# Performance work log

Hardware: AMD Instinct MI355X
Metric: run time of the kernel (lower is better)

The kernel has to match this reference:

```python
import jax, jax.numpy as jnp
import numpy as np

B, S_IMG, S_TXT, D, H, HD = 1, 4096, 512, 3072, 24, 128
EPS = 1e-5
SCALE = 1.0 / np.sqrt(HD)


def _linear(x, W, b=None):
    # torch nn.Linear: y = x @ W.T + b, W is [out, in]
    y = jnp.einsum('bsd,od->bso', x, W)
    return y if b is None else y + b


def _rmsnorm(x, w):
    # over last dim (head_dim), torch nn.RMSNorm with affine weight
    var = jnp.mean(jnp.square(x), axis=-1, keepdims=True)
    return x * jax.lax.rsqrt(var + EPS) * w


def _rope(x, cos, sin):
    # x: [B, S, H, D]; cos/sin: [S, D]; interleaved-pair rotation
    xr = x.reshape(*x.shape[:-1], HD // 2, 2)
    x_real, x_imag = xr[..., 0], xr[..., 1]
    x_rot = jnp.stack([-x_imag, x_real], axis=-1).reshape(x.shape)
    return x * cos[None, :, None, :] + x_rot * sin[None, :, None, :]


def setup_inputs() -> dict:
    key = jax.random.key(0)
    ks = jax.random.split(key, 24)
    s = 0.02
    inp = {
        'hidden_states': jax.random.normal(ks[0], (B, S_IMG, D), jnp.float32),
        'encoder_hidden_states': jax.random.normal(ks[1], (B, S_TXT, D), jnp.float32),
        'rope_cos': jax.random.uniform(ks[2], (S_IMG + S_TXT, HD), jnp.float32),
        'rope_sin': jax.random.uniform(ks[3], (S_IMG + S_TXT, HD), jnp.float32),
        # image-stream qkv (bias=False)
        'Wq': jax.random.normal(ks[4], (D, D), jnp.float32) * s,
        'Wk': jax.random.normal(ks[5], (D, D), jnp.float32) * s,
        'Wv': jax.random.normal(ks[6], (D, D), jnp.float32) * s,
        # text-stream qkv (bias=True)
        'Waq': jax.random.normal(ks[7], (D, D), jnp.float32) * s,
        'baq': jnp.zeros((D,), jnp.float32),
        'Wak': jax.random.normal(ks[8], (D, D), jnp.float32) * s,
        'bak': jnp.zeros((D,), jnp.float32),
        'Wav': jax.random.normal(ks[9], (D, D), jnp.float32) * s,
        'bav': jnp.zeros((D,), jnp.float32),
        # output projections (bias=True)
        'Wo': jax.random.normal(ks[10], (D, D), jnp.float32) * s,
        'bo': jnp.zeros((D,), jnp.float32),
        'Wao': jax.random.normal(ks[11], (D, D), jnp.float32) * s,
        'bao': jnp.zeros((D,), jnp.float32),
        # RMSNorm weights on head_dim
        'wq_norm': jnp.ones((HD,), jnp.float32),
        'wk_norm': jnp.ones((HD,), jnp.float32),
        'waq_norm': jnp.ones((HD,), jnp.float32),
        'wak_norm': jnp.ones((HD,), jnp.float32),
    }
    return inp


def reference(hidden_states, encoder_hidden_states, rope_cos, rope_sin,
              Wq, Wk, Wv, Waq, baq, Wak, bak, Wav, bav,
              Wo, bo, Wao, bao, wq_norm, wk_norm, waq_norm, wak_norm):
    # image-stream qkv -> [B, S_img, H, HD]
    q = _linear(hidden_states, Wq).reshape(B, S_IMG, H, HD)
    k = _linear(hidden_states, Wk).reshape(B, S_IMG, H, HD)
    v = _linear(hidden_states, Wv).reshape(B, S_IMG, H, HD)
    q = _rmsnorm(q, wq_norm)
    k = _rmsnorm(k, wk_norm)
    # text-stream qkv -> [B, S_txt, H, HD]
    eq = _linear(encoder_hidden_states, Waq, baq).reshape(B, S_TXT, H, HD)
    ek = _linear(encoder_hidden_states, Wak, bak).reshape(B, S_TXT, H, HD)
    ev = _linear(encoder_hidden_states, Wav, bav).reshape(B, S_TXT, H, HD)
    eq = _rmsnorm(eq, waq_norm)
    ek = _rmsnorm(ek, wak_norm)
    # concat [encoder, image] along sequence
    q = jnp.concatenate([eq, q], axis=1)  # [B, S_total, H, HD]
    k = jnp.concatenate([ek, k], axis=1)
    v = jnp.concatenate([ev, v], axis=1)
    # RoPE on joint sequence
    q = _rope(q, rope_cos, rope_sin)
    k = _rope(k, rope_cos, rope_sin)
    # SDPA over joint sequence
    scores = jnp.einsum('bqhd,bkhd->bhqk', q, k) * SCALE
    probs = jax.nn.softmax(scores, axis=-1)
    out = jnp.einsum('bhqk,bkhd->bqhd', probs, v)  # [B, S_total, H, HD]
    out = out.reshape(B, S_IMG + S_TXT, D)
    enc_out = _linear(out[:, :S_TXT], Wao, bao)
    img_out = _linear(out[:, S_TXT:], Wo, bo)
    return (img_out, enc_out)
```

## Files before the change

### kernel.cpp

```cpp
#include <hip/hip_runtime.h>

typedef __bf16 bf16_t;
typedef __bf16 bf16x8 __attribute__((ext_vector_type(8)));
typedef float  f32x4  __attribute__((ext_vector_type(4)));

#define S_IMG 4096
#define S_TXT 512
#define S_TOT 4608
#define DMODEL 3072
#define NH 24
#define HD 128

__device__ __forceinline__ void load_lds16(const void* g, void* l) {
  __builtin_amdgcn_global_load_lds(
      (const __attribute__((address_space(1))) void*)g,
      (__attribute__((address_space(3))) void*)l, 16, 0, 0);
}

#define BARRIER() do { asm volatile("" ::: "memory");                          \
                       __builtin_amdgcn_s_barrier();                           \
                       asm volatile("" ::: "memory"); } while (0)

__global__ __launch_bounds__(256) void f2b_kernel(const float* __restrict__ in,
                                                  bf16_t* __restrict__ out, int n) {
  int i = (blockIdx.x * 256 + threadIdx.x) * 4;
  if (i >= n) return;
  float4 v = *(const float4*)(in + i);
  union { bf16_t b[4]; uint2 u; } pk;
  pk.b[0] = (bf16_t)v.x; pk.b[1] = (bf16_t)v.y;
  pk.b[2] = (bf16_t)v.z; pk.b[3] = (bf16_t)v.w;
  *(uint2*)(out + i) = pk.u;
}

template <typename OT>
__global__ __launch_bounds__(512, 2) void gemm256(
    const bf16_t* __restrict__ A0, const bf16_t* __restrict__ B0,
    OT* __restrict__ C0, const float* __restrict__ bias0, int mt0,
    const bf16_t* __restrict__ A1, const bf16_t* __restrict__ B1,
    OT* __restrict__ C1, const float* __restrict__ bias1, int swzq)
{
  const int NT = DMODEL / 64;
  __shared__ bf16_t As[2][2][256 * 32];
  __shared__ bf16_t Bs[2][2][256 * 32];

  int bid = blockIdx.x;
  int t = (bid & 7) * swzq + (bid >> 3);
  int nb0 = mt0 * 12;
  const bf16_t* A; const bf16_t* B; OT* C; const float* bias;
  if (t < nb0) { A = A0; B = B0; C = C0; bias = bias0; }
  else { t -= nb0; A = A1; B = B1; C = C1; bias = bias1; }
  int bx = t % 12, by = t / 12;

  int tid = threadIdx.x;
  int lane = tid & 63, wid = tid >> 6;
  int l15 = lane & 15, lg = lane >> 4;
  int wm = wid >> 2, wn = wid & 3;

  const bf16_t* Ag = A + (size_t)by * 256 * DMODEL;
  const bf16_t* Bg = B + (size_t)bx * 256 * DMODEL;

  int ur0 = tid >> 2;
  int uc0 = (tid & 3) * 8;

  auto stage = [&](int ht) {
    int T = ht >> 2, sl = ht & 3, kh = sl >> 1;
    const bf16_t* G = (sl & 1) ? Bg : Ag;
    bf16_t* L = (sl & 1) ? &Bs[T & 1][kh][0] : &As[T & 1][kh][0];
    int kbase = T * 64 + kh * 32;
    #pragma unroll
    for (int j = 0; j < 2; j++) {
      int r = j * 128 + ur0;
      load_lds16(G + (size_t)r * DMODEL + kbase + uc0,
                 (char*)L + (size_t)(j * 512 + tid) * 16);
    }
  };

  f32x4 acc[8][4];
  f32x4 zero = {0.f, 0.f, 0.f, 0.f};
  #pragma unroll
  for (int m = 0; m < 8; m++)
    #pragma unroll
    for (int n = 0; n < 4; n++) acc[m][n] = zero;

  stage(0); stage(1); stage(2); stage(3); stage(4); stage(5);
  asm volatile("s_waitcnt vmcnt(8)" ::: "memory");
  BARRIER();

  for (int T = 0; T < NT; ++T) {
    int cur = T & 1;
    const bf16_t* A0s = &As[cur][0][0];
    const bf16_t* A1s = &As[cur][1][0];
    const bf16_t* B0s = &Bs[cur][0][0];
    const bf16_t* B1s = &Bs[cur][1][0];
    bf16x8 af[4], bfr[4];

    #pragma unroll
    for (int n = 0; n < 4; n++)
      bfr[n] = *(const bf16x8*)(B0s + (wn * 64 + n * 16 + l15) * 32 + lg * 8);
    #pragma unroll
    for (int m = 0; m < 4; m++)
      af[m] = *(const bf16x8*)(A0s + (wm * 128 + m * 16 + l15) * 32 + lg * 8);
    if (T + 1 < NT) stage(4 * T + 6);
    BARRIER();
    __builtin_amdgcn_s_setprio(1);
    #pragma unroll
    for (int m = 0; m < 4; m++)
      #pragma unroll
      for (int n = 0; n < 4; n++)
        acc[m][n] = __builtin_amdgcn_mfma_f32_16x16x32_bf16(af[m], bfr[n], acc[m][n], 0, 0, 0);
    __builtin_amdgcn_s_setprio(0);
    BARRIER();

    #pragma unroll
    for (int m = 0; m < 4; m++)
      af[m] = *(const bf16x8*)(A0s + (wm * 128 + 64 + m * 16 + l15) * 32 + lg * 8);
    if (T + 1 < NT) stage(4 * T + 7);
    BARRIER();
    __builtin_amdgcn_s_setprio(1);
    #pragma unroll
    for (int m = 0; m < 4; m++)
      #pragma unroll
      for (int n = 0; n < 4; n++)
        acc[4 + m][n] = __builtin_amdgcn_mfma_f32_16x16x32_bf16(af[m], bfr[n], acc[4 + m][n], 0, 0, 0);
    __builtin_amdgcn_s_setprio(0);
    if (T < NT - 1) asm volatile("s_waitcnt vmcnt(8)" ::: "memory");
    else            asm volatile("s_waitcnt vmcnt(0)" ::: "memory");
    BARRIER();

    #pragma unroll
    for (int n = 0; n < 4; n++)
      bfr[n] = *(const bf16x8*)(B1s + (wn * 64 + n * 16 + l15) * 32 + lg * 8);
    #pragma unroll
    for (int m = 0; m < 4; m++)
      af[m] = *(const bf16x8*)(A1s + (wm * 128 + m * 16 + l15) * 32 + lg * 8);
    if (T + 2 < NT) stage(4 * T + 8);
    BARRIER();
    __builtin_amdgcn_s_setprio(1);
    #pragma unroll
    for (int m = 0; m < 4; m++)
      #pragma unroll
      for (int n = 0; n < 4; n++)
        acc[m][n] = __builtin_amdgcn_mfma_f32_16x16x32_bf16(af[m], bfr[n], acc[m][n], 0, 0, 0);
    __builtin_amdgcn_s_setprio(0);
    BARRIER();

    #pragma unroll
    for (int m = 0; m < 4; m++)
      af[m] = *(const bf16x8*)(A1s + (wm * 128 + 64 + m * 16 + l15) * 32 + lg * 8);
    if (T + 2 < NT) stage(4 * T + 9);
    BARRIER();
    __builtin_amdgcn_s_setprio(1);
    #pragma unroll
    for (int m = 0; m < 4; m++)
      #pragma unroll
      for (int n = 0; n < 4; n++)
        acc[4 + m][n] = __builtin_amdgcn_mfma_f32_16x16x32_bf16(af[m], bfr[n], acc[4 + m][n], 0, 0, 0);
    __builtin_amdgcn_s_setprio(0);
    if (T < NT - 2)      asm volatile("s_waitcnt vmcnt(8)" ::: "memory");
    else if (T == NT - 2) asm volatile("s_waitcnt vmcnt(4)" ::: "memory");
    BARRIER();
  }

  size_t row0 = (size_t)by * 256 + wm * 128;
  int col0 = bx * 256 + wn * 64;
  #pragma unroll
  for (int n = 0; n < 4; n++) {
    int col = col0 + n * 16 + l15;
    float bv = bias ? bias[col] : 0.f;
    #pragma unroll
    for (int m = 0; m < 8; m++) {
      #pragma unroll
      for (int r = 0; r < 4; r++) {
        size_t row = row0 + m * 16 + lg * 4 + r;
        C[row * DMODEL + col] = (OT)(acc[m][n][r] + bv);
      }
    }
  }
}

__global__ __launch_bounds__(256) void qk_post(
    const bf16_t* __restrict__ qbuf, const bf16_t* __restrict__ kbuf,
    const float* __restrict__ cosb, const float* __restrict__ sinb,
    const float* __restrict__ wqn, const float* __restrict__ wkn,
    const float* __restrict__ waqn, const float* __restrict__ wakn,
    bf16_t* __restrict__ Qh, bf16_t* __restrict__ Kh)
{
  int gw = blockIdx.x * 4 + (threadIdx.x >> 6);
  int lane = threadIdx.x & 63;
  int s = gw / NH, h = gw - (gw / NH) * NH;
  if (s >= S_TOT) return;
  int d0 = lane * 2;
  const bf16_t* qp = qbuf + (size_t)s * DMODEL + h * HD + d0;
  const bf16_t* kp = kbuf + (size_t)s * DMODEL + h * HD + d0;
  float q0 = (float)qp[0], q1 = (float)qp[1];
  float k0 = (float)kp[0], k1 = (float)kp[1];
  float sq = q0 * q0 + q1 * q1, sk = k0 * k0 + k1 * k1;
  #pragma unroll
  for (int m = 1; m < 64; m <<= 1) { sq += __shfl_xor(sq, m); sk += __shfl_xor(sk, m); }
  float rq = rsqrtf(sq * (1.f / HD) + 1e-5f);
  float rk = rsqrtf(sk * (1.f / HD) + 1e-5f);
  const float* qn = (s < S_TXT) ? waqn : wqn;
  const float* kn = (s < S_TXT) ? wakn : wkn;
  q0 *= rq * qn[d0]; q1 *= rq * qn[d0 + 1];
  k0 *= rk * kn[d0]; k1 *= rk * kn[d0 + 1];
  float c0 = cosb[s * HD + d0], c1 = cosb[s * HD + d0 + 1];
  float s0 = sinb[s * HD + d0], s1 = sinb[s * HD + d0 + 1];
  const float SCALE = 0.1275174319942397f;
  float oq0 = (q0 * c0 - q1 * s0) * SCALE;
  float oq1 = (q1 * c1 + q0 * s1) * SCALE;
  float ok0 = k0 * c0 - k1 * s0;
  float ok1 = k1 * c1 + k0 * s1;
  size_t ob = ((size_t)h * S_TOT + s) * HD + d0;
  union { bf16_t b[2]; unsigned int u; } pq, pk;
  pq.b[0] = (bf16_t)oq0; pq.b[1] = (bf16_t)oq1;
  pk.b[0] = (bf16_t)ok0; pk.b[1] = (bf16_t)ok1;
  *(unsigned int*)(Qh + ob) = pq.u;
  *(unsigned int*)(Kh + ob) = pk.u;
}

__global__ __launch_bounds__(256) void v_trans(const bf16_t* __restrict__ vbuf,
                                               bf16_t* __restrict__ Vt) {
  __shared__ bf16_t tile[64 * 130];
  int h = blockIdx.y, s0 = blockIdx.x * 64;
  int tid = threadIdx.x;
  #pragma unroll
  for (int i = 0; i < 16; i++) {
    int idx = tid + i * 256;
    int sr = idx >> 6, dp = idx & 63;
    unsigned int u = *(const unsigned int*)(vbuf + (size_t)(s0 + sr) * DMODEL + h * HD + dp * 2);
    *(unsigned int*)&tile[sr * 130 + dp * 2] = u;
  }
  __syncthreads();
  #pragma unroll
  for (int i = 0; i < 16; i++) {
    int idx = tid + i * 256;
    int d = idx >> 5, scp = idx & 31;
    union { bf16_t b[2]; unsigned int u; } pk;
    pk.b[0] = tile[(scp * 2) * 130 + d];
    pk.b[1] = tile[(scp * 2 + 1) * 130 + d];
    *(unsigned int*)(Vt + ((size_t)h * HD + d) * S_TOT + s0 + scp * 2) = pk.u;
  }
}

__global__ __launch_bounds__(256, 2) void attn_kernel(
    const bf16_t* __restrict__ Qh, const bf16_t* __restrict__ Kh,
    const bf16_t* __restrict__ Vt, bf16_t* __restrict__ O)
{
  int bid = blockIdx.x;
  int orig = (bid & 7) * 108 + (bid >> 3);
  int h = orig / 36;
  int q0 = (orig % 36) * 128;

  int tid = threadIdx.x, w = tid >> 6, lane = tid & 63;
  int l15 = lane & 15, lg = lane >> 4;
  int sw = (l15 & 7) << 4;

  __shared__ bf16_t Ks[2][64 * 128];
  __shared__ bf16_t Vs[2][128 * 64];
  __shared__ bf16_t Ps[4][32 * 64];

  const bf16_t* Kbase = Kh + (size_t)h * S_TOT * HD;
  const bf16_t* Vbase = Vt + (size_t)h * HD * S_TOT;
  bf16_t* Pw = &Ps[w][0];

  bf16x8 qf[2][4];
  #pragma unroll
  for (int qh = 0; qh < 2; qh++) {
    const bf16_t* Qrow = Qh + ((size_t)h * S_TOT + q0 + w * 32 + qh * 16 + l15) * HD + lg * 8;
    #pragma unroll
    for (int dc = 0; dc < 4; dc++) qf[qh][dc] = *(const bf16x8*)(Qrow + dc * 32);
  }

  f32x4 o[2][8];
  f32x4 zero = {0.f, 0.f, 0.f, 0.f};
  #pragma unroll
  for (int qh = 0; qh < 2; qh++)
    #pragma unroll
    for (int i = 0; i < 8; i++) o[qh][i] = zero;
  float m0 = -1e30f, m1 = -1e30f, l0 = 0.f, l1 = 0.f;

#define STAGE(buf, kt) do {                                                    \
    _Pragma("unroll")                                                          \
    for (int i_ = 0; i_ < 4; i_++) {                                           \
      int Lb = (tid + i_ * 256) * 16; int row = Lb >> 8, cb = Lb & 255;        \
      int sb = cb ^ ((row & 7) << 4);                                          \
      load_lds16(Kbase + (size_t)((kt) + row) * HD + (sb >> 1),                \
                 (char*)Ks[buf] + Lb);                                         \
    }                                                                          \
    _Pragma("unroll")                                                          \
    for (int i_ = 0; i_ < 4; i_++) {                                           \
      int Lb = (tid + i_ * 256) * 16; int row = Lb >> 7, cb = Lb & 127;        \
      int sb = cb ^ ((row & 7) << 4);                                          \
      load_lds16(Vbase + (size_t)row * S_TOT + (kt) + (sb >> 1),               \
                 (char*)Vs[buf] + Lb);                                         \
    }                                                                          \
  } while (0)

  STAGE(0, 0);
  __syncthreads();

  const int NT = S_TOT / 64;
  for (int t = 0; t < NT; ++t) {
    int cur = t & 1;
    if (t + 1 < NT) STAGE(cur ^ 1, (t + 1) * 64);

    f32x4 sacc[2][4];
    #pragma unroll
    for (int qh = 0; qh < 2; qh++)
      #pragma unroll
      for (int c = 0; c < 4; c++) sacc[qh][c] = zero;
    const char* Kc = (const char*)Ks[cur];
    #pragma unroll
    for (int c = 0; c < 4; c++) {
      int row = c * 16 + l15;
      int rs = (row & 7) << 4;
      const char* kr = Kc + row * 256;
      #pragma unroll
      for (int dc = 0; dc < 4; dc++) {
        bf16x8 kf = *(const bf16x8*)(kr + ((dc * 64 + lg * 16) ^ rs));
        sacc[0][c] = __builtin_amdgcn_mfma_f32_16x16x32_bf16(kf, qf[0][dc], sacc[0][c], 0, 0, 0);
        sacc[1][c] = __builtin_amdgcn_mfma_f32_16x16x32_bf16(kf, qf[1][dc], sacc[1][c], 0, 0, 0);
      }
    }

    float px0 = sacc[0][0][0], px1 = sacc[1][0][0];
    #pragma unroll
    for (int c = 0; c < 4; c++)
      #pragma unroll
      for (int r = 0; r < 4; r++) {
        px0 = fmaxf(px0, sacc[0][c][r]);
        px1 = fmaxf(px1, sacc[1][c][r]);
      }
    px0 = fmaxf(px0, __shfl_xor(px0, 16)); px0 = fmaxf(px0, __shfl_xor(px0, 32));
    px1 = fmaxf(px1, __shfl_xor(px1, 16)); px1 = fmaxf(px1, __shfl_xor(px1, 32));

    bool need = (px0 > m0 + 8.f) || (px1 > m1 + 8.f);
    if (__any(need)) {
      float mn0 = fmaxf(m0, px0), mn1 = fmaxf(m1, px1);
      float a0 = exp2f(m0 - mn0), a1 = exp2f(m1 - mn1);
      m0 = mn0; m1 = mn1; l0 *= a0; l1 *= a1;
      #pragma unroll
      for (int r = 0; r < 4; r++) {
        float f0 = __shfl(a0, lg * 4 + r);
        float f1 = __shfl(a1, lg * 4 + r);
        #pragma unroll
        for (int dn = 0; dn < 8; dn++) { o[0][dn][r] *= f0; o[1][dn][r] *= f1; }
      }
    }

    #pragma unroll
    for (int qh = 0; qh < 2; qh++) {
      float m = qh ? m1 : m0;
      float rsum = 0.f;
      char* Prow = (char*)Pw + (qh * 16 + l15) * 128;
      #pragma unroll
      for (int c = 0; c < 4; c++) {
        union { bf16_t b[4]; uint2 u; } pk;
        #pragma unroll
        for (int r = 0; r < 4; r++) {
          float p = exp2f(sacc[qh][c][r] - m);
          rsum += p;
          pk.b[r] = (bf16_t)p;
        }
        *(uint2*)(Prow + ((c * 32 + lg * 8) ^ sw)) = pk.u;
      }
      rsum += __shfl_xor(rsum, 16);
      rsum += __shfl_xor(rsum, 32);
      if (qh) l1 += rsum; else l0 += rsum;
    }

    bf16x8 pf[2][2];
    #pragma unroll
    for (int qh = 0; qh < 2; qh++) {
      const char* Prow = (const char*)Pw + (qh * 16 + l15) * 128;
      #pragma unroll
      for (int kc = 0; kc < 2; kc++)
        pf[qh][kc] = *(const bf16x8*)(Prow + ((kc * 64 + lg * 16) ^ sw));
    }
    const char* Vc = (const char*)Vs[cur];
    #pragma unroll
    for (int dn = 0; dn < 8; dn++) {
      int row = dn * 16 + l15;
      int rs2 = (row & 7) << 4;
      const char* vr = Vc + row * 128;
      bf16x8 vf0 = *(const bf16x8*)(vr + ((lg * 16) ^ rs2));
      bf16x8 vf1 = *(const bf16x8*)(vr + ((64 + lg * 16) ^ rs2));
      o[0][dn] = __builtin_amdgcn_mfma_f32_16x16x32_bf16(pf[0][0], vf0, o[0][dn], 0, 0, 0);
      o[0][dn] = __builtin_amdgcn_mfma_f32_16x16x32_bf16(pf[0][1], vf1, o[0][dn], 0, 0, 0);
      o[1][dn] = __builtin_amdgcn_mfma_f32_16x16x32_bf16(pf[1][0], vf0, o[1][dn], 0, 0, 0);
      o[1][dn] = __builtin_amdgcn_mfma_f32_16x16x32_bf16(pf[1][1], vf1, o[1][dn], 0, 0, 0);
    }

    __syncthreads();
  }
#undef STAGE

  #pragma unroll
  for (int qh = 0; qh < 2; qh++) {
    #pragma unroll
    for (int r = 0; r < 4; r++) {
      float lv = __shfl(qh ? l1 : l0, lg * 4 + r);
      float inv = 1.f / lv;
      size_t srow = (size_t)q0 + w * 32 + qh * 16 + lg * 4 + r;
      #pragma unroll
      for (int dn = 0; dn < 8; dn++)
        O[srow * DMODEL + h * HD + dn * 16 + l15] = (bf16_t)(o[qh][dn][r] * inv);
    }
  }
}

extern "C" void kernel_launch(void* const* d_in, const int* in_sizes, int n_in,
                              void* d_out, int out_size, void* d_ws, size_t ws_size,
                              hipStream_t stream) {
  const float* hidden = (const float*)d_in[0];
  const float* enc    = (const float*)d_in[1];
  const float* ropec  = (const float*)d_in[2];
  const float* ropes  = (const float*)d_in[3];
  const float* Wq  = (const float*)d_in[4];
  const float* Wk  = (const float*)d_in[5];
  const float* Wv  = (const float*)d_in[6];
  const float* Waq = (const float*)d_in[7];
  const float* baq = (const float*)d_in[8];
  const float* Wak = (const float*)d_in[9];
  const float* bak = (const float*)d_in[10];
  const float* Wav = (const float*)d_in[11];
  const float* bav = (const float*)d_in[12];
  const float* Wo  = (const float*)d_in[13];
  const float* bo  = (const float*)d_in[14];
  const float* Wao = (const float*)d_in[15];
  const float* bao = (const float*)d_in[16];
  const float* wqn = (const float*)d_in[17];
  const float* wkn = (const float*)d_in[18];
  const float* waqn = (const float*)d_in[19];
  const float* wakn = (const float*)d_in[20];

  const size_t WSZ = (size_t)DMODEL * DMODEL;
  const size_t SEQSZ = (size_t)S_TOT * DMODEL;
  if (ws_size < (2 * WSZ + 6 * SEQSZ) * sizeof(bf16_t)) return;

  bf16_t* s0   = (bf16_t*)d_ws;
  bf16_t* s1   = s0 + WSZ;
  bf16_t* xbi  = s1 + WSZ;
  bf16_t* xbt  = xbi + (size_t)S_IMG * DMODEL;
  bf16_t* qbuf = xbi + SEQSZ;
  bf16_t* kbuf = qbuf + SEQSZ;
  bf16_t* vbuf = kbuf + SEQSZ;
  bf16_t* Kh   = vbuf + SEQSZ;
  bf16_t* Vh   = Kh + SEQSZ;
  bf16_t* Qh   = xbi;
  bf16_t* attn_o = qbuf;
  float* outf = (float*)d_out;

  f2b_kernel<<<S_IMG * DMODEL / 1024, 256, 0, stream>>>(hidden, xbi, S_IMG * DMODEL);
  f2b_kernel<<<S_TXT * DMODEL / 1024, 256, 0, stream>>>(enc, xbt, S_TXT * DMODEL);

  const int WB = (int)(WSZ / 1024);
  f2b_kernel<<<WB, 256, 0, stream>>>(Wq,  s0, (int)WSZ);
  f2b_kernel<<<WB, 256, 0, stream>>>(Waq, s1, (int)WSZ);
  gemm256<bf16_t><<<216, 512, 0, stream>>>(
      xbi, s0, qbuf + (size_t)S_TXT * DMODEL, nullptr, 16,
      xbt, s1, qbuf, baq, 27);
  f2b_kernel<<<WB, 256, 0, stream>>>(Wk,  s0, (int)WSZ);
  f2b_kernel<<<WB, 256, 0, stream>>>(Wak, s1, (int)WSZ);
  gemm256<bf16_t><<<216, 512, 0, stream>>>(
      xbi, s0, kbuf + (size_t)S_TXT * DMODEL, nullptr, 16,
      xbt, s1, kbuf, bak, 27);
  f2b_kernel<<<WB, 256, 0, stream>>>(Wv,  s0, (int)WSZ);
  f2b_kernel<<<WB, 256, 0, stream>>>(Wav, s1, (int)WSZ);
  gemm256<bf16_t><<<216, 512, 0, stream>>>(
      xbi, s0, vbuf + (size_t)S_TXT * DMODEL, nullptr, 16,
      xbt, s1, vbuf, bav, 27);

  qk_post<<<S_TOT * NH / 4, 256, 0, stream>>>(qbuf, kbuf, ropec, ropes,
                                              wqn, wkn, waqn, wakn, Qh, Kh);
  v_trans<<<dim3(S_TOT / 64, NH), 256, 0, stream>>>(vbuf, Vh);

  attn_kernel<<<36 * 24, 256, 0, stream>>>(Qh, Kh, Vh, attn_o);

  f2b_kernel<<<WB, 256, 0, stream>>>(Wo,  s0, (int)WSZ);
  f2b_kernel<<<WB, 256, 0, stream>>>(Wao, s1, (int)WSZ);
  gemm256<float><<<216, 512, 0, stream>>>(
      attn_o + (size_t)S_TXT * DMODEL, s0, outf, bo, 16,
      attn_o, s1, outf + (size_t)S_IMG * DMODEL, bao, 27);
}
```

Measured before the change: 1.007 ms.

## Swizzle GEMM LDS, single-buffer attention K/V with split staging, merge weight casts

The GEMM now XOR-swizzles the 16-byte chunk column in both the async global-to-LDS stores and the fragment reads, to reduce LDS bank conflicts. The attention kernel drops K/V double buffering for single buffers, issuing the next K load after QK^T and the next V load after PV, and raises launch bounds to 3 blocks per CU because it now uses less LDS. Weight fp32-to-bf16 casts for each pair of projections are merged into one launch. Single buffering exposes more load latency per iteration, which the higher occupancy is meant to hide.

```diff
diff --git a/kernel.cpp b/kernel.cpp
--- a/kernel.cpp
+++ b/kernel.cpp
@@ -25,6 +25,20 @@
                                                   bf16_t* __restrict__ out, int n) {
   int i = (blockIdx.x * 256 + threadIdx.x) * 4;
   if (i >= n) return;
+  float4 v = *(const float4*)(in + i);
+  union { bf16_t b[4]; uint2 u; } pk;
+  pk.b[0] = (bf16_t)v.x; pk.b[1] = (bf16_t)v.y;
+  pk.b[2] = (bf16_t)v.z; pk.b[3] = (bf16_t)v.w;
+  *(uint2*)(out + i) = pk.u;
+}
+
+__global__ __launch_bounds__(256) void f2b2_kernel(
+    const float* __restrict__ in0, bf16_t* __restrict__ out0,
+    const float* __restrict__ in1, bf16_t* __restrict__ out1, int nb) {
+  int b = blockIdx.x;
+  const float* in = (b < nb) ? in0 : in1;
+  bf16_t* out = (b < nb) ? out0 : out1;
+  int i = (((b < nb) ? b : b - nb) * 256 + threadIdx.x) * 4;
   float4 v = *(const float4*)(in + i);
   union { bf16_t b[4]; uint2 u; } pk;
   pk.b[0] = (bf16_t)v.x; pk.b[1] = (bf16_t)v.y;
@@ -55,12 +69,13 @@
   int lane = tid & 63, wid = tid >> 6;
   int l15 = lane & 15, lg = lane >> 4;
   int wm = wid >> 2, wn = wid & 3;
+  int sx = (lg ^ ((l15 >> 1) & 3)) * 8;
 
   const bf16_t* Ag = A + (size_t)by * 256 * DMODEL;
   const bf16_t* Bg = B + (size_t)bx * 256 * DMODEL;
 
   int ur0 = tid >> 2;
-  int uc0 = (tid & 3) * 8;
+  int uc0 = ((tid & 3) ^ ((tid >> 3) & 3)) * 8;
 
   auto stage = [&](int ht) {
     int T = ht >> 2, sl = ht & 3, kh = sl >> 1;
@@ -96,10 +111,10 @@
 
     #pragma unroll
     for (int n = 0; n < 4; n++)
-      bfr[n] = *(const bf16x8*)(B0s + (wn * 64 + n * 16 + l15) * 32 + lg * 8);
-    #pragma unroll
-    for (int m = 0; m < 4; m++)
-      af[m] = *(const bf16x8*)(A0s + (wm * 128 + m * 16 + l15) * 32 + lg * 8);
+      bfr[n] = *(const bf16x8*)(B0s + (wn * 64 + n * 16 + l15) * 32 + sx);
+    #pragma unroll
+    for (int m = 0; m < 4; m++)
+      af[m] = *(const bf16x8*)(A0s + (wm * 128 + m * 16 + l15) * 32 + sx);
     if (T + 1 < NT) stage(4 * T + 6);
     BARRIER();
     __builtin_amdgcn_s_setprio(1);
@@ -113,7 +128,7 @@
 
     #pragma unroll
     for (int m = 0; m < 4; m++)
-      af[m] = *(const bf16x8*)(A0s + (wm * 128 + 64 + m * 16 + l15) * 32 + lg * 8);
+      af[m] = *(const bf16x8*)(A0s + (wm * 128 + 64 + m * 16 + l15) * 32 + sx);
     if (T + 1 < NT) stage(4 * T + 7);
     BARRIER();
     __builtin_amdgcn_s_setprio(1);
@@ -129,10 +144,10 @@
 
     #pragma unroll
     for (int n = 0; n < 4; n++)
-      bfr[n] = *(const bf16x8*)(B1s + (wn * 64 + n * 16 + l15) * 32 + lg * 8);
-    #pragma unroll
-    for (int m = 0; m < 4; m++)
-      af[m] = *(const bf16x8*)(A1s + (wm * 128 + m * 16 + l15) * 32 + lg * 8);
+      bfr[n] = *(const bf16x8*)(B1s + (wn * 64 + n * 16 + l15) * 32 + sx);
+    #pragma unroll
+    for (int m = 0; m < 4; m++)
+      af[m] = *(const bf16x8*)(A1s + (wm * 128 + m * 16 + l15) * 32 + sx);
     if (T + 2 < NT) stage(4 * T + 8);
     BARRIER();
     __builtin_amdgcn_s_setprio(1);
@@ -146,7 +161,7 @@
 
     #pragma unroll
     for (int m = 0; m < 4; m++)
-      af[m] = *(const bf16x8*)(A1s + (wm * 128 + 64 + m * 16 + l15) * 32 + lg * 8);
+      af[m] = *(const bf16x8*)(A1s + (wm * 128 + 64 + m * 16 + l15) * 32 + sx);
     if (T + 2 < NT) stage(4 * T + 9);
     BARRIER();
     __builtin_amdgcn_s_setprio(1);
@@ -156,7 +171,7 @@
       for (int n = 0; n < 4; n++)
         acc[4 + m][n] = __builtin_amdgcn_mfma_f32_16x16x32_bf16(af[m], bfr[n], acc[4 + m][n], 0, 0, 0);
     __builtin_amdgcn_s_setprio(0);
-    if (T < NT - 2)      asm volatile("s_waitcnt vmcnt(8)" ::: "memory");
+    if (T < NT - 2)       asm volatile("s_waitcnt vmcnt(8)" ::: "memory");
     else if (T == NT - 2) asm volatile("s_waitcnt vmcnt(4)" ::: "memory");
     BARRIER();
   }
@@ -242,7 +257,7 @@
   }
 }
 
-__global__ __launch_bounds__(256, 2) void attn_kernel(
+__global__ __launch_bounds__(256, 3) void attn_kernel(
     const bf16_t* __restrict__ Qh, const bf16_t* __restrict__ Kh,
     const bf16_t* __restrict__ Vt, bf16_t* __restrict__ O)
 {
@@ -255,8 +270,8 @@
   int l15 = lane & 15, lg = lane >> 4;
   int sw = (l15 & 7) << 4;
 
-  __shared__ bf16_t Ks[2][64 * 128];
-  __shared__ bf16_t Vs[2][128 * 64];
+  __shared__ bf16_t Ks[64 * 128];
+  __shared__ bf16_t Vs[128 * 64];
   __shared__ bf16_t Ps[4][32 * 64];
 
   const bf16_t* Kbase = Kh + (size_t)h * S_TOT * HD;
@@ -270,6 +285,7 @@
     #pragma unroll
     for (int dc = 0; dc < 4; dc++) qf[qh][dc] = *(const bf16x8*)(Qrow + dc * 32);
   }
+  asm volatile("s_waitcnt vmcnt(0)" ::: "memory");
 
   f32x4 o[2][8];
   f32x4 zero = {0.f, 0.f, 0.f, 0.f};
@@ -279,47 +295,52 @@
     for (int i = 0; i < 8; i++) o[qh][i] = zero;
   float m0 = -1e30f, m1 = -1e30f, l0 = 0.f, l1 = 0.f;
 
-#define STAGE(buf, kt) do {                                                    \
+#define STAGE_K(kt) do {                                                       \
     _Pragma("unroll")                                                          \
-    for (int i_ = 0; i_ < 4; i_++) {                                           \
+    for (int i_ = 0; i_ < 4; i_++) {                    \
       int Lb = (tid + i_ * 256) * 16; int row = Lb >> 8, cb = Lb & 255;        \
       int sb = cb ^ ((row & 7) << 4);                                          \
       load_lds16(Kbase + (size_t)((kt) + row) * HD + (sb >> 1),                \
-                 (char*)Ks[buf] + Lb);                                         \
+                 (char*)Ks + Lb);                                              \
     }                                                                          \
+  } while (0)
+
+#define STAGE_V(kt) do {                                                       \
     _Pragma("unroll")                                                          \
-    for (int i_ = 0; i_ < 4; i_++) {                                           \
+    for (int i_ = 0; i_ < 4; i_++) {                   \
       int Lb = (tid + i_ * 256) * 16; int row = Lb >> 7, cb = Lb & 127;        \
       int sb = cb ^ ((row & 7) << 4);                                          \
       load_lds16(Vbase + (size_t)row * S_TOT + (kt) + (sb >> 1),               \
-                 (char*)Vs[buf] + Lb);                                         \
+                 (char*)Vs + Lb);                                              \
     }                                                                          \
   } while (0)
 
-  STAGE(0, 0);
-  __syncthreads();
+  STAGE_K(0);
+  STAGE_V(0);
 
   const int NT = S_TOT / 64;
   for (int t = 0; t < NT; ++t) {
-    int cur = t & 1;
-    if (t + 1 < NT) STAGE(cur ^ 1, (t + 1) * 64);
+    asm volatile("s_waitcnt vmcnt(4)" ::: "memory");
+    BARRIER();
 
     f32x4 sacc[2][4];
     #pragma unroll
     for (int qh = 0; qh < 2; qh++)
       #pragma unroll
       for (int c = 0; c < 4; c++) sacc[qh][c] = zero;
-    const char* Kc = (const char*)Ks[cur];
-    #pragma unroll
-    for (int c = 0; c < 4; c++) {
-      int row = c * 16 + l15;
-      int rs = (row & 7) << 4;
-      const char* kr = Kc + row * 256;
-      #pragma unroll
-      for (int dc = 0; dc < 4; dc++) {
-        bf16x8 kf = *(const bf16x8*)(kr + ((dc * 64 + lg * 16) ^ rs));
-        sacc[0][c] = __builtin_amdgcn_mfma_f32_16x16x32_bf16(kf, qf[0][dc], sacc[0][c], 0, 0, 0);
-        sacc[1][c] = __builtin_amdgcn_mfma_f32_16x16x32_bf16(kf, qf[1][dc], sacc[1][c], 0, 0, 0);
+    {
+      const char* Kc = (const char*)Ks;
+      #pragma unroll
+      for (int c = 0; c < 4; c++) {
+        int row = c * 16 + l15;
+        int rs = (row & 7) << 4;
+        const char* kr = Kc + row * 256;
+        #pragma unroll
+        for (int dc = 0; dc < 4; dc++) {
+          bf16x8 kf = *(const bf16x8*)(kr + ((dc * 64 + lg * 16) ^ rs));
+          sacc[0][c] = __builtin_amdgcn_mfma_f32_16x16x32_bf16(kf, qf[0][dc], sacc[0][c], 0, 0, 0);
+          sacc[1][c] = __builtin_amdgcn_mfma_f32_16x16x32_bf16(kf, qf[1][dc], sacc[1][c], 0, 0, 0);
+        }
       }
     }
 
@@ -368,7 +389,6 @@
       rsum += __shfl_xor(rsum, 32);
       if (qh) l1 += rsum; else l0 += rsum;
     }
-
     bf16x8 pf[2][2];
     #pragma unroll
     for (int qh = 0; qh < 2; qh++) {
@@ -377,23 +397,32 @@
       for (int kc = 0; kc < 2; kc++)
         pf[qh][kc] = *(const bf16x8*)(Prow + ((kc * 64 + lg * 16) ^ sw));
     }
-    const char* Vc = (const char*)Vs[cur];
-    #pragma unroll
-    for (int dn = 0; dn < 8; dn++) {
-      int row = dn * 16 + l15;
-      int rs2 = (row & 7) << 4;
-      const char* vr = Vc + row * 128;
-      bf16x8 vf0 = *(const bf16x8*)(vr + ((lg * 16) ^ rs2));
-      bf16x8 vf1 = *(const bf16x8*)(vr + ((64 + lg * 16) ^ rs2));
-      o[0][dn] = __builtin_amdgcn_mfma_f32_16x16x32_bf16(pf[0][0], vf0, o[0][dn], 0, 0, 0);
-      o[0][dn] = __builtin_amdgcn_mfma_f32_16x16x32_bf16(pf[0][1], vf1, o[0][dn], 0, 0, 0);
-      o[1][dn] = __builtin_amdgcn_mfma_f32_16x16x32_bf16(pf[1][0], vf0, o[1][dn], 0, 0, 0);
-      o[1][dn] = __builtin_amdgcn_mfma_f32_16x16x32_bf16(pf[1][1], vf1, o[1][dn], 0, 0, 0);
-    }
-
-    __syncthreads();
-  }
-#undef STAGE
+
+    asm volatile("s_waitcnt vmcnt(0)" ::: "memory");
+    BARRIER();
+    if (t + 1 < NT) STAGE_K((t + 1) * 64);
+
+    {
+      const char* Vc = (const char*)Vs;
+      #pragma unroll
+      for (int dn = 0; dn < 8; dn++) {
+        int row = dn * 16 + l15;
+        int rs2 = (row & 7) << 4;
+        const char* vr = Vc + row * 128;
+        bf16x8 vf0 = *(const bf16x8*)(vr + ((lg * 16) ^ rs2));
+        bf16x8 vf1 = *(const bf16x8*)(vr + ((64 + lg * 16) ^ rs2));
+        o[0][dn] = __builtin_amdgcn_mfma_f32_16x16x32_bf16(pf[0][0], vf0, o[0][dn], 0, 0, 0);
+        o[0][dn] = __builtin_amdgcn_mfma_f32_16x16x32_bf16(pf[0][1], vf1, o[0][dn], 0, 0, 0);
+        o[1][dn] = __builtin_amdgcn_mfma_f32_16x16x32_bf16(pf[1][0], vf0, o[1][dn], 0, 0, 0);
+        o[1][dn] = __builtin_amdgcn_mfma_f32_16x16x32_bf16(pf[1][1], vf1, o[1][dn], 0, 0, 0);
+      }
+    }
+
+    BARRIER();
+    if (t + 1 < NT) STAGE_V((t + 1) * 64);
+  }
+#undef STAGE_K
+#undef STAGE_V
 
   #pragma unroll
   for (int qh = 0; qh < 2; qh++) {
@@ -455,18 +484,15 @@
   f2b_kernel<<<S_TXT * DMODEL / 1024, 256, 0, stream>>>(enc, xbt, S_TXT * DMODEL);
 
   const int WB = (int)(WSZ / 1024);
-  f2b_kernel<<<WB, 256, 0, stream>>>(Wq,  s0, (int)WSZ);
-  f2b_kernel<<<WB, 256, 0, stream>>>(Waq, s1, (int)WSZ);
+  f2b2_kernel<<<2 * WB, 256, 0, stream>>>(Wq, s0, Waq, s1, WB);
   gemm256<bf16_t><<<216, 512, 0, stream>>>(
       xbi, s0, qbuf + (size_t)S_TXT * DMODEL, nullptr, 16,
       xbt, s1, qbuf, baq, 27);
-  f2b_kernel<<<WB, 256, 0, stream>>>(Wk,  s0, (int)WSZ);
-  f2b_kernel<<<WB, 256, 0, stream>>>(Wak, s1, (int)WSZ);
+  f2b2_kernel<<<2 * WB, 256, 0, stream>>>(Wk, s0, Wak, s1, WB);
   gemm256<bf16_t><<<216, 512, 0, stream>>>(
       xbi, s0, kbuf + (size_t)S_TXT * DMODEL, nullptr, 16,
       xbt, s1, kbuf, bak, 27);
-  f2b_kernel<<<WB, 256, 0, stream>>>(Wv,  s0, (int)WSZ);
-  f2b_kernel<<<WB, 256, 0, stream>>>(Wav, s1, (int)WSZ);
+  f2b2_kernel<<<2 * WB, 256, 0, stream>>>(Wv, s0, Wav, s1, WB);
   gemm256<bf16_t><<<216, 512, 0, stream>>>(
       xbi, s0, vbuf + (size_t)S_TXT * DMODEL, nullptr, 16,
       xbt, s1, vbuf, bav, 27);
@@ -477,8 +503,7 @@
 
   attn_kernel<<<36 * 24, 256, 0, stream>>>(Qh, Kh, Vh, attn_o);
 
-  f2b_kernel<<<WB, 256, 0, stream>>>(Wo,  s0, (int)WSZ);
-  f2b_kernel<<<WB, 256, 0, stream>>>(Wao, s1, (int)WSZ);
+  f2b2_kernel<<<2 * WB, 256, 0, stream>>>(Wo, s0, Wao, s1, WB);
   gemm256<float><<<216, 512, 0, stream>>>(
       attn_o + (size_t)S_TXT * DMODEL, s0, outf, bo, 16,
       attn_o, s1, outf + (size_t)S_IMG * DMODEL, bao, 27);
```

Result: slower. 1.234 ms (+22.4%).
